# Optimization experiments

Hardware: AMD Instinct MI355X
Metric: run time of the kernel (lower is better)

Reference implementation:

```python
import math
import jax, jax.numpy as jnp
import numpy as np

FNUM = 64      # exp_channels (fnum)
NHEADS = 4     # num_heads
WS = 8         # window size (both spatial dims)
SHIFT = 4      # cyclic shift (hard-coded in module)
SCALE = FNUM ** -0.5   # NOTE: module scales by fnum**-0.5, not head_dim**-0.5
LN_EPS = 1e-5


def sine_pos_encoding(h, w, num_pos_feats, temperature=10000.0):
    # DETR-style normalized sine position encoding -> (1, h*w, 2*num_pos_feats)
    scale = 2.0 * math.pi
    y = np.cumsum(np.ones((1, h, w), dtype=np.float64), axis=1)
    x = np.cumsum(np.ones((1, h, w), dtype=np.float64), axis=2)
    eps = 1e-6
    y = y / (y[:, -1:, :] + eps) * scale
    x = x / (x[:, :, -1:] + eps) * scale
    dim_t = np.arange(num_pos_feats, dtype=np.float64)
    dim_t = temperature ** (2.0 * (dim_t // 2) / num_pos_feats)
    pos_x = x[..., None] / dim_t
    pos_y = y[..., None] / dim_t
    pos_x = np.stack([np.sin(pos_x[..., 0::2]), np.cos(pos_x[..., 1::2])], axis=-1).reshape(1, h, w, -1)
    pos_y = np.stack([np.sin(pos_y[..., 0::2]), np.cos(pos_y[..., 1::2])], axis=-1).reshape(1, h, w, -1)
    pos = np.concatenate([pos_y, pos_x], axis=-1)
    return jnp.asarray(pos.reshape(1, h * w, 2 * num_pos_feats), dtype=jnp.float32)


def compute_mask_np(H, W, ws, ss):
    # Swin shifted-window attention mask -> (nW, ws*ws, ws*ws) with 0 / -100
    img = np.zeros((H, W))
    cnt = 0
    for hs in (slice(0, -ws), slice(-ws, -ss), slice(-ss, None)):
        for wsl in (slice(0, -ws), slice(-ws, -ss), slice(-ss, None)):
            img[hs, wsl] = cnt
            cnt += 1
    mw = img.reshape(H // ws, ws, W // ws, ws).transpose(0, 2, 1, 3).reshape(-1, ws * ws)
    diff = mw[:, None, :] - mw[:, :, None]
    return jnp.asarray(np.where(diff != 0, -100.0, 0.0), dtype=jnp.float32)


def layernorm(x, w, b):
    m = x.mean(-1, keepdims=True)
    v = x.var(-1, keepdims=True)
    return (x - m) * jax.lax.rsqrt(v + LN_EPS) * w + b


def window_attention(q, k, v, mask):
    # q,k,v: (Bw, nH, N, Ch); mask: (nW, N, N)
    att = jnp.einsum('bhnc,bhmc->bhnm', q * SCALE, k)
    nW, N = mask.shape[0], mask.shape[1]
    att = att.reshape(-1, nW, NHEADS, N, N) + mask[None, :, None]
    att = jax.nn.softmax(att.reshape(-1, NHEADS, N, N), axis=-1)
    out = jnp.einsum('bhnm,bhmc->bnhc', att, v)   # merge heads as (nH C)
    return out.reshape(out.shape[0], N, -1)


def merge_heads(q):
    # (Bw, nH, N, Ch) -> (Bw, N, nH*Ch)
    return q.transpose(0, 2, 1, 3).reshape(q.shape[0], q.shape[2], -1)


def geglu(h, w11, b11, w12, b12, w2, b2):
    return (jax.nn.gelu(h @ w11 + b11, approximate=False) * (h @ w12 + b12)) @ w2 + b2


def reference(x, ln1_w, ln1_b, ln2_w, ln2_b, w_qkv, me_w11, me_b11, me_w12, me_b12, me_w2, me_b2, conv11_w, ff_in_w, ff_dw_w, ff_out_w):
    B, _, C, H, W = x.shape
    nHw, nWw = H // WS, W // WS
    nW = nHw * nWw
    N = WS * WS
    Ch = FNUM // NHEADS
    pos = sine_pos_encoding(WS, WS, FNUM // 2)
    mask = compute_mask_np(H, W, WS, SHIFT)
    x0 = x
    xs = jnp.roll(x, (-SHIFT, -SHIFT), axis=(3, 4))
    # window partition: (B,3,C,H,W) -> (B*3*nW, N, C)
    xw = xs.reshape(B, 3, C, nHw, WS, nWw, WS).transpose(0, 1, 3, 5, 4, 6, 2).reshape(-1, N, C)
    xw = layernorm(xw, ln1_w, ln1_b)
    qkv = (xw + pos) @ w_qkv                                   # (B*3*nW, N, 3F)
    # '(B E nW) W (nP C) -> E nP (B nW) W C'
    qkv = qkv.reshape(B, 3, nW, N, 3, FNUM).transpose(1, 4, 0, 2, 3, 5).reshape(3, 3, B * nW, N, FNUM)
    # '(C nH)' head split: head index is the fast axis (faithful to source)
    qkv = qkv.reshape(3, 3, B * nW, N, Ch, NHEADS).transpose(0, 1, 2, 5, 3, 4)  # (E, P, Bw, nH, N, Ch)
    a1 = window_attention(qkv[1, 0], qkv[0, 1], qkv[0, 2], mask)
    a3 = window_attention(qkv[1, 0], qkv[2, 1], qkv[2, 2], mask)
    a21 = window_attention(qkv[0, 0], qkv[1, 1], qkv[1, 2], mask)
    a21b = window_attention(qkv[0, 0], qkv[2, 1], qkv[2, 2], mask)
    a23 = window_attention(qkv[2, 0], qkv[1, 1], qkv[1, 2], mask)
    a23b = window_attention(qkv[2, 0], qkv[0, 1], qkv[0, 2], mask)
    # keep_query=True path: concat attended features with own query, GEGLU per exposure
    h1 = geglu(jnp.concatenate([a21, a21b, merge_heads(qkv[0, 0])], -1), me_w11[0], me_b11[0], me_w12[0], me_b12[0], me_w2[0], me_b2[0])
    h2 = geglu(jnp.concatenate([a1, a3, merge_heads(qkv[1, 0])], -1), me_w11[1], me_b11[1], me_w12[1], me_b12[1], me_w2[1], me_b2[1])
    h3 = geglu(jnp.concatenate([a23, a23b, merge_heads(qkv[2, 0])], -1), me_w11[2], me_b11[2], me_w12[2], me_b12[2], me_w2[2], me_b2[2])
    xc = jnp.concatenate([h1, h2, h3], 0)                      # (3*B*nW, N, F)
    # window reverse + ffn_dconv 1x1 conv across 3F channels
    xr = xc.reshape(3, B, nHw, nWw, WS, WS, FNUM).transpose(1, 0, 6, 2, 4, 3, 5).reshape(B, 3 * FNUM, H, W)
    xr = jnp.einsum('oi,bihw->bohw', conv11_w, xr).reshape(B, 3, FNUM, H, W)
    xr = jnp.roll(xr, (SHIFT, SHIFT), axis=(3, 4))
    xres = xr + x0
    # FFN: LN over (N C), then GEGLU dwconv FeedForward
    xl = layernorm(xres.transpose(0, 3, 4, 1, 2).reshape(B, H, W, 3 * FNUM), ln2_w, ln2_b)
    xcn = xl.transpose(0, 3, 1, 2)                             # (B, 3F, H, W)
    h = jnp.einsum('oi,bihw->bohw', ff_in_w, xcn)              # (B, 12F, H, W)
    h = jax.lax.conv_general_dilated(h, ff_dw_w[:, None], (1, 1), ((1, 1), (1, 1)),
                                     feature_group_count=h.shape[1],
                                     dimension_numbers=('NCHW', 'OIHW', 'NCHW'))
    g1, g2 = jnp.split(h, 2, axis=1)
    h = jax.nn.gelu(g1, approximate=False) * g2                # (B, 6F, H, W)
    out = jnp.einsum('oi,bihw->bohw', ff_out_w, h).reshape(B, 3, FNUM, H, W)
    return xres + out


def setup_inputs():
    key = jax.random.key(0)
    ks = jax.random.split(key, 10)
    F3, F6, F12 = 3 * FNUM, 6 * FNUM, 12 * FNUM
    def w(k, shape, fan_in):
        return jax.random.normal(k, shape, jnp.float32) * (fan_in ** -0.5)
    return {
        'x': jax.random.normal(ks[0], (1, 3, FNUM, 256, 256), jnp.float32),
        'ln1_w': jnp.ones((FNUM,), jnp.float32),
        'ln1_b': jnp.zeros((FNUM,), jnp.float32),
        'ln2_w': jnp.ones((F3,), jnp.float32),
        'ln2_b': jnp.zeros((F3,), jnp.float32),
        'w_qkv': w(ks[1], (FNUM, F3), FNUM),
        'me_w11': w(ks[2], (3, F3, FNUM), F3),
        'me_b11': jnp.zeros((3, FNUM), jnp.float32),
        'me_w12': w(ks[3], (3, F3, FNUM), F3),
        'me_b12': jnp.zeros((3, FNUM), jnp.float32),
        'me_w2': w(ks[4], (3, FNUM, FNUM), FNUM),
        'me_b2': jnp.zeros((3, FNUM), jnp.float32),
        'conv11_w': w(ks[5], (F3, F3), F3),
        'ff_in_w': w(ks[6], (F12, F3), F3),
        'ff_dw_w': w(ks[7], (F12, 3, 3), 9),
        'ff_out_w': w(ks[8], (F3, F6), F6),
    }
```

## Files before the change

### kernel.cpp

```cpp
#include <hip/hip_runtime.h>
#include <hip/hip_bf16.h>
#include <math.h>

typedef __hip_bfloat16 bf16;
typedef __attribute__((ext_vector_type(8))) short short8;
typedef __attribute__((ext_vector_type(4))) short short4v;
typedef __attribute__((ext_vector_type(4))) float f32x4;

__device__ __forceinline__ float b2f(bf16 v) { return __bfloat162float(v); }
__device__ __forceinline__ bf16 f2b(float v) { return __float2bfloat16(v); }
__device__ __forceinline__ short f2s(float v) { bf16 b = __float2bfloat16(v); return *(short*)&b; }
__device__ __forceinline__ float s2f(short s) { bf16 b = *(bf16*)&s; return __bfloat162float(b); }
__device__ __forceinline__ float gelu_fast(float x) {
  float z = 0.7978845608028654f * x * (1.0f + 0.044715f * x * x);
  float e = __expf(2.0f * z);
  float t = 1.0f - 2.0f / (e + 1.0f);
  return 0.5f * x * (1.0f + t);
}
__device__ __forceinline__ bool detect_f32(const void* ln1w) {
  return *(const unsigned int*)ln1w == 0x3F800000u;
}
__device__ __forceinline__ float ldx(const void* p, int i, bool f32) {
  return f32 ? ((const float*)p)[i] : b2f(((const bf16*)p)[i]);
}
#define MFMA16(a, b, c) __builtin_amdgcn_mfma_f32_16x16x32_bf16((a), (b), (c), 0, 0, 0)

#define OFF_LN1W  0
#define OFF_LN1B  64
#define OFF_LN2W  128
#define OFF_LN2B  320
#define OFF_WQKVT 512
#define OFF_W11T  12800
#define OFF_B11   49664
#define OFF_W12T  49856
#define OFF_B12   86720
#define OFF_W2T   86912
#define OFF_B2    99200
#define OFF_CW    99392
#define OFF_FIW   136256
#define OFF_DWW   283712
#define OFF_FOW   290624

#define QOFF 0
#define KOFF 4352
#define VOFF 9472

__global__ void __launch_bounds__(256) k_convert(
    const void* __restrict__ src, bf16* __restrict__ dst, int n,
    const void* __restrict__ raw) {
  const bool f32 = detect_f32(raw);
  int i = blockIdx.x * 256 + threadIdx.x;
  if (i < n) dst[i] = f2b(ldx(src, i, f32));
}

__global__ void __launch_bounds__(256) k_convT(
    const void* __restrict__ src, bf16* __restrict__ dst, int R, int C, int n,
    const void* __restrict__ raw) {
  const bool f32 = detect_f32(raw);
  int i = blockIdx.x * 256 + threadIdx.x;
  if (i >= n) return;
  int rc = R * C;
  int s = i / rc, rem = i - s * rc;
  int r = rem / C, c = rem - r * C;
  dst[s * rc + c * R + r] = f2b(ldx(src, i, f32));
}

__global__ void __launch_bounds__(256) k_pos(float* __restrict__ posT) {
  int i = blockIdx.x * 256 + threadIdx.x;
  if (i >= 4096) return;
  int t = i >> 6, ch = i & 63;
  int r = t >> 3, c = t & 7;
  int c2 = ch & 31;
  float coord = (ch < 32) ? (float)(r + 1) : (float)(c + 1);
  float base = coord * (6.283185307179586f / 8.000001f);
  int k = c2 >> 1;
  float d = powf(10000.0f, (float)k * (1.0f / 16.0f));
  float a = base / d;
  posT[i] = (c2 & 1) ? cosf(a) : sinf(a);
}

__global__ void __launch_bounds__(256) k_qkv(
    const void* __restrict__ x, const void* __restrict__ raw,
    const bf16* __restrict__ W, const float* __restrict__ posT,
    short* __restrict__ qkvS, int wy0, int NWL) {
  const int wl = blockIdx.x;
  const int wy = wy0 + (wl >> 5), wx = wl & 31;
  const int tid = threadIdx.x;
  const bool xf32 = detect_f32(raw);

  __shared__ alignas(16) short xln[192 * 72];
  __shared__ alignas(16) short qout[13824];
  __shared__ float mu[192], rs[192];

  for (int i = tid; i < 3072; i += 256) {
    int xq = i & 1, ty = (i >> 1) & 7, ch = (i >> 4) & 63, e = i >> 10;
    int y  = (wy * 8 + ty + 4) & 255;
    int xs = (wx * 8 + 4 + xq * 4) & 255;
    size_t gi = ((size_t)(e * 64 + ch) * 256 + y) * 256 + xs;
    float f0, f1, f2, f3;
    if (xf32) {
      f32x4 v4 = *(const f32x4*)((const float*)x + gi);
      f0 = v4[0]; f1 = v4[1]; f2 = v4[2]; f3 = v4[3];
    } else {
      short4v v4 = *(const short4v*)((const bf16*)x + gi);
      f0 = s2f(v4[0]); f1 = s2f(v4[1]); f2 = s2f(v4[2]); f3 = s2f(v4[3]);
    }
    int tb = (e * 64 + ty * 8 + xq * 4) * 72 + ch;
    xln[tb]       = f2s(f0);
    xln[tb + 72]  = f2s(f1);
    xln[tb + 144] = f2s(f2);
    xln[tb + 216] = f2s(f3);
  }
  __syncthreads();
  if (tid < 192) {
    const short* row = xln + tid * 72;
    float s = 0.f, s2 = 0.f;
    #pragma unroll
    for (int k8 = 0; k8 < 8; k8++) {
      short8 v = *(const short8*)(row + k8 * 8);
      #pragma unroll
      for (int j = 0; j < 8; j++) { float f = s2f(v[j]); s += f; s2 += f * f; }
    }
    float m = s * (1.0f / 64.0f);
    float var = s2 * (1.0f / 64.0f) - m * m;
    mu[tid] = m; rs[tid] = rsqrtf(var + 1e-5f);
  }
  __syncthreads();
  for (int u = tid; u < 1536; u += 256) {
    int co = u & 7, t = (u >> 3) & 63, e = u >> 9;
    int idx = (e * 64 + t) * 72 + co * 8;
    short8 xv = *(const short8*)(xln + idx);
    float m = mu[e * 64 + t], rr = rs[e * 64 + t];
    const float* pt = posT + t * 64 + co * 8;
    f32x4 pa = *(const f32x4*)pt;
    f32x4 pb = *(const f32x4*)(pt + 4);
    short8 lw = *(const short8*)(const void*)(W + OFF_LN1W + co * 8);
    short8 lb = *(const short8*)(const void*)(W + OFF_LN1B + co * 8);
    short8 o;
    #pragma unroll
    for (int j = 0; j < 8; j++) {
      float p = (j < 4) ? pa[j] : pb[j - 4];
      o[j] = f2s((s2f(xv[j]) - m) * rr * s2f(lw[j]) + s2f(lb[j]) + p);
    }
    *(short8*)(xln + idx) = o;
  }
  __syncthreads();

  const int lid = tid & 63;
  const int w = tid >> 6;
  const int mrow = lid & 15, q = lid >> 4;
  const int t0 = w * 16 + q * 4;
  const int h = mrow & 3;
  const bf16* wqT = W + OFF_WQKVT;
  for (int e = 0; e < 3; e++) {
    short8 a0 = *(const short8*)(xln + (e * 64 + w * 16 + mrow) * 72 + q * 8);
    short8 a1 = *(const short8*)(xln + (e * 64 + w * 16 + mrow) * 72 + 32 + q * 8);
    for (int nt = 0; nt < 12; nt++) {
      f32x4 acc = {0.f, 0.f, 0.f, 0.f};
      short8 b0 = *(const short8*)(const void*)(wqT + (nt * 16 + mrow) * 64 + q * 8);
      short8 b1 = *(const short8*)(const void*)(wqT + (nt * 16 + mrow) * 64 + 32 + q * 8);
      acc = MFMA16(a0, b0, acc);
      acc = MFMA16(a1, b1, acc);
      int p = nt >> 2;
      int c = (nt & 3) * 4 + (mrow >> 2);
      if (p == 0) {
        int o2 = h * 16 + c;
        #pragma unroll
        for (int r = 0; r < 4; r++)
          qout[QOFF + (t0 + r) * 68 + o2] = f2s(acc[r]);
      } else if (p == 1) {
        int rb = KOFF + (h * 64 + t0) * 20 + c;
        #pragma unroll
        for (int r = 0; r < 4; r++)
          qout[rb + r * 20] = f2s(acc[r] * 0.125f);
      } else {
        int rb = VOFF + (h * 16 + c) * 68 + q * 16 + w;
        #pragma unroll
        for (int r = 0; r < 4; r++)
          qout[rb + r * 4] = f2s(acc[r]);
      }
    }
    __syncthreads();
    const size_t gb = ((size_t)wl * 9 + e * 3) * 4096;
    for (int u = tid; u < 3072; u += 256) {
      int j = u * 4, p = j >> 12, rem = j & 4095, src;
      if (p == 0)      src = QOFF + (rem >> 6) * 68 + (rem & 63);
      else if (p == 1) src = KOFF + (rem >> 4) * 20 + (rem & 15);
      else             src = VOFF + (rem >> 6) * 68 + (rem & 63);
      *(short4v*)(qkvS + gb + j) = *(const short4v*)(qout + src);
    }
    __syncthreads();
  }
}

__global__ void __launch_bounds__(256, 3) k_attn(
    const short* __restrict__ qkvS, const bf16* __restrict__ W,
    short* __restrict__ xcS, int wy0, int NWL) {
  const int e  = blockIdx.x / NWL;
  const int wl = blockIdx.x - e * NWL;
  const int wy = wy0 + (wl >> 5), wx = wl & 31;
  const int tid = threadIdx.x;

  __shared__ alignas(16) short cat[64 * 200];
  __shared__ alignas(16) short Kh[4096];
  __shared__ alignas(16) short Vt[64 * 72];
  __shared__ alignas(16) short Pb[64 * 72];
  __shared__ alignas(16) short kz[16];
  short* gbuf = Pb;

  const int ea = (e == 0) ? 1 : ((e == 1) ? 0 : 1);
  const int eb = (e == 0) ? 2 : ((e == 1) ? 2 : 0);
  const short* Qg = qkvS + ((size_t)wl * 9 + e * 3 + 0) * 4096;
  const short* Kg[2] = { qkvS + ((size_t)wl * 9 + ea * 3 + 1) * 4096,
                         qkvS + ((size_t)wl * 9 + eb * 3 + 1) * 4096 };
  const short* Vg[2] = { qkvS + ((size_t)wl * 9 + ea * 3 + 2) * 4096,
                         qkvS + ((size_t)wl * 9 + eb * 3 + 2) * 4096 };

  if (tid < 16) kz[tid] = 0;
  for (int i = tid; i < 512; i += 256) {
    int t = i >> 3, ch = i & 7;
    *(short8*)(cat + t * 200 + 128 + ch * 8) = *(const short8*)(Qg + t * 64 + ch * 8);
  }

  const int lid = tid & 63;
  const int w = tid >> 6;
  const int mrow = lid & 15, q = lid >> 4;
  const int masky = (wy == 31), maskx = (wx == 31);
  const bool anymask = (masky | maskx) != 0;
  const short8 zero8 = {0, 0, 0, 0, 0, 0, 0, 0};

  float madd[4][4];
  if (anymask) {
    int qi = w * 16 + mrow;
    int lyi = masky ? (((qi >> 3) < 4) ? 1 : 2) : 0;
    int lxi = maskx ? (((qi & 7) < 4) ? 1 : 2) : 0;
    #pragma unroll
    for (int nt = 0; nt < 4; nt++)
      #pragma unroll
      for (int r = 0; r < 4; r++) {
        int kj = nt * 16 + q * 4 + r;
        int lyj = masky ? (((kj >> 3) < 4) ? 1 : 2) : 0;
        int lxj = maskx ? (((kj & 7) < 4) ? 1 : 2) : 0;
        madd[nt][r] = (lyi != lyj || lxi != lxj) ? -100.0f : 0.0f;
      }
  }

  for (int src = 0; src < 2; src++) {
    if (src) __syncthreads();
    for (int i = tid; i < 512; i += 256)
      *(short8*)(Kh + i * 8) = *(const short8*)(Kg[src] + i * 8);
    for (int i = tid; i < 512; i += 256) {
      int row = i >> 3, ch = i & 7;
      *(short8*)(Vt + row * 72 + ch * 8) = *(const short8*)(Vg[src] + row * 64 + ch * 8);
    }
    __syncthreads();

    for (int h = 0; h < 4; h++) {
      short8 qf = (q < 2)
          ? *(const short8*)(cat + (w * 16 + mrow) * 200 + 128 + h * 16 + q * 8)
          : zero8;
      const short* kb; int kstep;
      if (q < 2) { kb = Kh + (h * 64 + mrow) * 16 + q * 8; kstep = 256; }
      else       { kb = kz; kstep = 0; }
      f32x4 s[4];
      #pragma unroll
      for (int nt = 0; nt < 4; nt++) {
        short8 kf = *(const short8*)(kb + nt * kstep);
        f32x4 z = {0.f, 0.f, 0.f, 0.f};
        s[nt] = MFMA16(kf, qf, z);
      }
      if (anymask) {
        #pragma unroll
        for (int nt = 0; nt < 4; nt++)
          #pragma unroll
          for (int r = 0; r < 4; r++) s[nt][r] += madd[nt][r];
      }
      float mx = s[0][0];
      #pragma unroll
      for (int nt = 0; nt < 4; nt++)
        #pragma unroll
        for (int r = 0; r < 4; r++) if (nt | r) mx = fmaxf(mx, s[nt][r]);
      mx = fmaxf(mx, __shfl_xor(mx, 16));
      mx = fmaxf(mx, __shfl_xor(mx, 32));
      float pr[4][4]; float sum = 0.f;
      #pragma unroll
      for (int nt = 0; nt < 4; nt++)
        #pragma unroll
        for (int r = 0; r < 4; r++) {
          float ev = __expf(s[nt][r] - mx);
          pr[nt][r] = ev; sum += ev;
        }
      sum += __shfl_xor(sum, 16);
      sum += __shfl_xor(sum, 32);
      float inv = 1.0f / sum;
      int ro = (w * 16 + mrow) * 72 + q * 16;
      #pragma unroll
      for (int r = 0; r < 4; r++) {
        short4v pv = { f2s(pr[0][r] * inv), f2s(pr[1][r] * inv),
                       f2s(pr[2][r] * inv), f2s(pr[3][r] * inv) };
        *(short4v*)(Pb + ro + r * 4) = pv;
      }
      asm volatile("s_waitcnt lgkmcnt(0)" ::: "memory");
      f32x4 o = {0.f, 0.f, 0.f, 0.f};
      #pragma unroll
      for (int kc = 0; kc < 2; kc++) {
        short8 pa = *(const short8*)(Pb + (w * 16 + mrow) * 72 + kc * 32 + q * 8);
        short8 vb = *(const short8*)(Vt + (h * 16 + mrow) * 72 + kc * 32 + q * 8);
        o = MFMA16(pa, vb, o);
      }
      #pragma unroll
      for (int r = 0; r < 4; r++)
        cat[(w * 16 + q * 4 + r) * 200 + src * 64 + h * 16 + mrow] = f2s(o[r]);
    }
  }
  __syncthreads();

  {
    short8 a[6];
    #pragma unroll
    for (int kc = 0; kc < 6; kc++)
      a[kc] = *(const short8*)(cat + (w * 16 + mrow) * 200 + kc * 32 + q * 8);
    f32x4 ua[4], va[4];
    const bf16* w1T = W + OFF_W11T + (size_t)e * 64 * 192;
    const bf16* w2T = W + OFF_W12T + (size_t)e * 64 * 192;
    for (int nt = 0; nt < 4; nt++) {
      f32x4 au = {0.f, 0.f, 0.f, 0.f}, av = {0.f, 0.f, 0.f, 0.f};
      #pragma unroll
      for (int kc = 0; kc < 6; kc++) {
        short8 bu = *(const short8*)(const void*)(w1T + (nt * 16 + mrow) * 192 + kc * 32 + q * 8);
        short8 bv = *(const short8*)(const void*)(w2T + (nt * 16 + mrow) * 192 + kc * 32 + q * 8);
        au = MFMA16(a[kc], bu, au);
        av = MFMA16(a[kc], bv, av);
      }
      ua[nt] = au; va[nt] = av;
    }
    for (int nt = 0; nt < 4; nt++) {
      int o = nt * 16 + mrow;
      float bu = b2f(W[OFF_B11 + e * 64 + o]);
      float bv = b2f(W[OFF_B12 + e * 64 + o]);
      #pragma unroll
      for (int r = 0; r < 4; r++)
        gbuf[(w * 16 + q * 4 + r) * 72 + o] = f2s(gelu_fast(ua[nt][r] + bu) * (va[nt][r] + bv));
    }
  }
  {
    short8 g0 = *(const short8*)(gbuf + (w * 16 + mrow) * 72 + q * 8);
    short8 g1 = *(const short8*)(gbuf + (w * 16 + mrow) * 72 + 32 + q * 8);
    const bf16* w2T = W + OFF_W2T + (size_t)e * 64 * 64;
    for (int nt = 0; nt < 4; nt++) {
      f32x4 acc = {0.f, 0.f, 0.f, 0.f};
      short8 b0 = *(const short8*)(const void*)(w2T + (nt * 16 + mrow) * 64 + q * 8);
      short8 b1 = *(const short8*)(const void*)(w2T + (nt * 16 + mrow) * 64 + 32 + q * 8);
      acc = MFMA16(g0, b0, acc);
      acc = MFMA16(g1, b1, acc);
      int o = nt * 16 + mrow;
      float bb = b2f(W[OFF_B2 + e * 64 + o]);
      #pragma unroll
      for (int r = 0; r < 4; r++)
        cat[(w * 16 + q * 4 + r) * 200 + o] = f2s(acc[r] + bb);
    }
  }
  __syncthreads();
  short* xcbase = xcS + ((size_t)wl * 3 + e) * 4096;
  for (int i = tid; i < 1024; i += 256) {
    int tt = i >> 4, f4 = (i & 15) * 4;
    *(short4v*)(xcbase + tt * 64 + f4) = *(const short4v*)(cat + tt * 200 + f4);
  }
}

__global__ void __launch_bounds__(256) k_conv11(
    const short* __restrict__ xcS, const bf16* __restrict__ W,
    const void* __restrict__ x, const void* __restrict__ raw,
    short* __restrict__ xres, int wy0, int NWL) {
  const int wl = blockIdx.x;
  const int wy = wy0 + (wl >> 5), wx = wl & 31;
  const int tid = threadIdx.x;
  const bool xf32 = detect_f32(raw);
  __shared__ alignas(16) short ct[64 * 200];
  __shared__ alignas(16) short xt[64 * 200];

  for (int i = tid; i < 3072; i += 256) {
    int e = i >> 10, rem = i & 1023;
    int tt = rem >> 4, f4 = (rem & 15) * 4;
    *(short4v*)(ct + tt * 200 + e * 64 + f4)
        = *(const short4v*)(xcS + ((size_t)wl * 3 + e) * 4096 + tt * 64 + f4);
  }
  for (int i = tid; i < 3072; i += 256) {
    int xq = i & 1, ty = (i >> 1) & 7, ch = (i >> 4) & 63, e = i >> 10;
    int y  = (wy * 8 + ty + 4) & 255;
    int xs = (wx * 8 + 4 + xq * 4) & 255;
    size_t gi = ((size_t)(e * 64 + ch) * 256 + y) * 256 + xs;
    float f0, f1, f2, f3;
    if (xf32) {
      f32x4 v4 = *(const f32x4*)((const float*)x + gi);
      f0 = v4[0]; f1 = v4[1]; f2 = v4[2]; f3 = v4[3];
    } else {
      short4v v4 = *(const short4v*)((const bf16*)x + gi);
      f0 = s2f(v4[0]); f1 = s2f(v4[1]); f2 = s2f(v4[2]); f3 = s2f(v4[3]);
    }
    int tb = (ty * 8 + xq * 4) * 200 + e * 64 + ch;
    xt[tb]       = f2s(f0);
    xt[tb + 200] = f2s(f1);
    xt[tb + 400] = f2s(f2);
    xt[tb + 600] = f2s(f3);
  }
  __syncthreads();

  const int lid = tid & 63;
  const int w = tid >> 6;
  const int mrow = lid & 15, q = lid >> 4;
  short8 a[6];
  #pragma unroll
  for (int kc = 0; kc < 6; kc++)
    a[kc] = *(const short8*)(ct + (w * 16 + mrow) * 200 + kc * 32 + q * 8);
  __syncthreads();

  const bf16* cw = W + OFF_CW;
  for (int nt = 0; nt < 12; nt++) {
    f32x4 acc = {0.f, 0.f, 0.f, 0.f};
    #pragma unroll
    for (int kc = 0; kc < 6; kc++) {
      short8 b = *(const short8*)(const void*)(cw + (nt * 16 + mrow) * 192 + kc * 32 + q * 8);
      acc = MFMA16(a[kc], b, acc);
    }
    int o = nt * 16 + mrow;
    #pragma unroll
    for (int r = 0; r < 4; r++) {
      int t = w * 16 + q * 4 + r;
      ct[t * 200 + o] = f2s(acc[r] + s2f(xt[t * 200 + o]));
    }
  }
  __syncthreads();
  for (int i4 = tid; i4 < 3072; i4 += 256) {
    int t = i4 / 48, o4 = (i4 - t * 48) * 4;
    int y  = (wy * 8 + (t >> 3) + 4) & 255;
    int xx = (wx * 8 + (t & 7) + 4) & 255;
    *(short4v*)(xres + (size_t)(y * 256 + xx) * 192 + o4)
        = *(const short4v*)(ct + t * 200 + o4);
  }
}

__global__ void __launch_bounds__(256) k_ffin(
    const short* __restrict__ xres, const bf16* __restrict__ W,
    short* __restrict__ hS, int y_start, int y0m1) {
  const int y = y_start + (blockIdx.x >> 2);
  const int x0 = (blockIdx.x & 3) * 64;
  const int l = y - y0m1;
  const int tid = threadIdx.x;
  __shared__ alignas(16) short xt[64 * 200];
  __shared__ float mu[64], rs[64];

  for (int i4 = tid; i4 < 3072; i4 += 256) {
    int p = i4 / 48, c4 = (i4 - p * 48) * 4;
    *(short4v*)(xt + p * 200 + c4)
        = *(const short4v*)(xres + (size_t)(y * 256 + x0 + p) * 192 + c4);
  }
  __syncthreads();
  {
    int p = tid >> 2, qd = tid & 3;
    const short* row = xt + p * 200 + qd * 48;
    float s = 0.f, s2 = 0.f;
    #pragma unroll
    for (int k = 0; k < 6; k++) {
      short8 v = *(const short8*)(row + k * 8);
      #pragma unroll
      for (int j = 0; j < 8; j++) { float f = s2f(v[j]); s += f; s2 += f * f; }
    }
    s  += __shfl_xor(s, 1);  s  += __shfl_xor(s, 2);
    s2 += __shfl_xor(s2, 1); s2 += __shfl_xor(s2, 2);
    if (qd == 0) {
      float m = s * (1.0f / 192.0f);
      float var = s2 * (1.0f / 192.0f) - m * m;
      mu[p] = m; rs[p] = rsqrtf(var + 1e-5f);
    }
  }
  __syncthreads();
  for (int i = tid; i < 12288; i += 256) {
    int p = i & 63, ch = i >> 6;
    int idx = p * 200 + ch;
    xt[idx] = f2s((s2f(xt[idx]) - mu[p]) * rs[p] * b2f(W[OFF_LN2W + ch]) + b2f(W[OFF_LN2B + ch]));
  }
  __syncthreads();

  const int lid = tid & 63;
  const int m0 = (tid >> 6) * 16;
  const int mrow = lid & 15, q = lid >> 4;
  short8 a[6];
  #pragma unroll
  for (int kc = 0; kc < 6; kc++)
    a[kc] = *(const short8*)(xt + (m0 + mrow) * 200 + kc * 32 + q * 8);
  __syncthreads();

  const bf16* fiw = W + OFF_FIW;
  for (int c = 0; c < 4; c++) {
    for (int j = 0; j < 12; j++) {
      int nt = c * 12 + j;
      f32x4 acc = {0.f, 0.f, 0.f, 0.f};
      #pragma unroll
      for (int kc = 0; kc < 6; kc++) {
        short8 b = *(const short8*)(const void*)(fiw + (nt * 16 + mrow) * 192 + kc * 32 + q * 8);
        acc = MFMA16(a[kc], b, acc);
      }
      #pragma unroll
      for (int r = 0; r < 4; r++)
        xt[(m0 + q * 4 + r) * 200 + j * 16 + mrow] = f2s(acc[r]);
    }
    __syncthreads();
    for (int i4 = tid; i4 < 3072; i4 += 256) {
      int t = i4 / 48, o4 = (i4 - t * 48) * 4;
      *(short4v*)(hS + (size_t)l * 196608 + (size_t)(x0 + t) * 768 + c * 192 + o4)
          = *(const short4v*)(xt + t * 200 + o4);
    }
    __syncthreads();
  }
}

__global__ void __launch_bounds__(256) k_ffout(
    const short* __restrict__ hS, const bf16* __restrict__ W,
    const short* __restrict__ xres, void* __restrict__ out,
    const void* __restrict__ raw, int y0, int y0m1) {
  const int y = y0 + (blockIdx.x >> 2);
  const int x0 = (blockIdx.x & 3) * 64;
  const int tid = threadIdx.x;
  const bool of32 = detect_f32(raw);
  __shared__ alignas(16) short ga[64 * 392];

  const bf16* dwwT = W + OFF_DWW;
  const int l = y - y0m1;
  const short8 z8 = {0, 0, 0, 0, 0, 0, 0, 0};
  for (int it = 0; it < 6; it++) {
    int unit = it * 256 + tid;
    int pq = unit / 48, oo = unit - pq * 48;
    int o = oo * 8;
    int xxb = x0 + pq * 2;
    float u0[8] = {0,0,0,0,0,0,0,0}, v0[8] = {0,0,0,0,0,0,0,0};
    float u1[8] = {0,0,0,0,0,0,0,0}, v1[8] = {0,0,0,0,0,0,0,0};
    #pragma unroll
    for (int dy = -1; dy <= 1; dy++) {
      int yy = y + dy;
      if (yy < 0 || yy >= 256) continue;
      const short* rbase = hS + (size_t)(l + dy) * 196608;
      short8 hu[4], hv[4];
      #pragma unroll
      for (int k = 0; k < 4; k++) {
        int xv = xxb - 1 + k;
        if (xv < 0 || xv >= 256) { hu[k] = z8; hv[k] = z8; }
        else {
          const short* hp = rbase + (size_t)xv * 768 + o;
          hu[k] = *(const short8*)(hp);
          hv[k] = *(const short8*)(hp + 384);
        }
      }
      const bf16* wrow = dwwT + (dy + 1) * 3 * 768 + o;
      short8 w0u = *(const short8*)(const void*)(wrow);
      short8 w0v = *(const short8*)(const void*)(wrow + 384);
      short8 w1u = *(const short8*)(const void*)(wrow + 768);
      short8 w1v = *(const short8*)(const void*)(wrow + 768 + 384);
      short8 w2u = *(const short8*)(const void*)(wrow + 1536);
      short8 w2v = *(const short8*)(const void*)(wrow + 1536 + 384);
      #pragma unroll
      for (int j = 0; j < 8; j++) {
        float a0 = s2f(w0u[j]), a1 = s2f(w1u[j]), a2 = s2f(w2u[j]);
        float b0 = s2f(w0v[j]), b1 = s2f(w1v[j]), b2 = s2f(w2v[j]);
        float h0u = s2f(hu[0][j]), h1u = s2f(hu[1][j]), h2u = s2f(hu[2][j]), h3u = s2f(hu[3][j]);
        float h0v = s2f(hv[0][j]), h1v = s2f(hv[1][j]), h2v = s2f(hv[2][j]), h3v = s2f(hv[3][j]);
        u0[j] += a0 * h0u + a1 * h1u + a2 * h2u;
        u1[j] += a0 * h1u + a1 * h2u + a2 * h3u;
        v0[j] += b0 * h0v + b1 * h1v + b2 * h2v;
        v1[j] += b0 * h1v + b1 * h2v + b2 * h3v;
      }
    }
    short8 g0, g1;
    #pragma unroll
    for (int j = 0; j < 8; j++) {
      g0[j] = f2s(gelu_fast(u0[j]) * v0[j]);
      g1[j] = f2s(gelu_fast(u1[j]) * v1[j]);
    }
    *(short8*)(ga + (pq * 2) * 392 + o)     = g0;
    *(short8*)(ga + (pq * 2 + 1) * 392 + o) = g1;
  }
  __syncthreads();

  const int lid = tid & 63;
  const int m0 = (tid >> 6) * 16;
  const int mrow = lid & 15, q = lid >> 4;
  short8 a[12];
  #pragma unroll
  for (int kc = 0; kc < 12; kc++)
    a[kc] = *(const short8*)(ga + (m0 + mrow) * 392 + kc * 32 + q * 8);
  __syncthreads();

  for (int i4 = tid; i4 < 3072; i4 += 256) {
    int pp = i4 / 48, c4 = (i4 - pp * 48) * 4;
    *(short4v*)(ga + pp * 392 + 200 + c4)
        = *(const short4v*)(xres + (size_t)(y * 256 + x0 + pp) * 192 + c4);
  }

  const bf16* fow = W + OFF_FOW;
  for (int nt = 0; nt < 12; nt++) {
    f32x4 acc = {0.f, 0.f, 0.f, 0.f};
    #pragma unroll
    for (int kc = 0; kc < 12; kc++) {
      short8 b = *(const short8*)(const void*)(fow + (nt * 16 + mrow) * 384 + kc * 32 + q * 8);
      acc = MFMA16(a[kc], b, acc);
    }
    #pragma unroll
    for (int r = 0; r < 4; r++)
      ga[(m0 + q * 4 + r) * 392 + nt * 16 + mrow] = f2s(acc[r]);
  }
  __syncthreads();

  for (int it = 0; it < 48; it++) {
    int flat = it * 256 + tid;
    int pp = flat & 63, ch = flat >> 6;
    int idx = ch * 65536 + y * 256 + x0 + pp;
    float r = s2f(ga[pp * 392 + ch]) + s2f(ga[pp * 392 + 200 + ch]);
    if (of32) ((float*)out)[idx] = r;
    else      ((bf16*)out)[idx] = f2b(r);
  }
}

extern "C" void kernel_launch(void* const* d_in, const int* in_sizes, int n_in,
                              void* d_out, int out_size, void* d_ws, size_t ws_size,
                              hipStream_t stream) {
  const void* x   = d_in[0];
  const void* raw = d_in[1];
  char* ws = (char*)d_ws;
  bf16*  W    = (bf16*)(ws + 1024);
  float* posT = (float*)(ws + 786432);
  short* xres = (short*)(ws + 0x100000);
  const size_t ATT = 28ull * 1024 * 1024;

  size_t avail = (ws_size > ATT) ? ws_size - ATT : 0;
  int swr = 32;
  while (swr > 1 && (size_t)swr * 3145728ull > avail) swr >>= 1;
  int hr = 256;
  while (hr > 4 && (size_t)(hr + 2) * 393216ull > avail) hr >>= 1;

  short* qkvS = (short*)(ws + ATT);
  short* xcS  = (short*)(ws + ATT + (size_t)swr * 2359296ull);
  short* hS   = (short*)(ws + ATT);

  { const int di[10]   = {1, 2, 3, 4, 7, 9, 11, 12, 13, 15};
    const int offp[10] = {OFF_LN1W, OFF_LN1B, OFF_LN2W, OFF_LN2B, OFF_B11,
                          OFF_B12, OFF_B2, OFF_CW, OFF_FIW, OFF_FOW};
    const int cnt[10]  = {64, 64, 192, 192, 192, 192, 192, 36864, 147456, 73728};
    for (int i = 0; i < 10; i++)
      k_convert<<<(cnt[i] + 255) / 256, 256, 0, stream>>>(
          d_in[di[i]], W + offp[i], cnt[i], raw);
  }
  k_convT<<<(12288 + 255) / 256, 256, 0, stream>>>(d_in[5], W + OFF_WQKVT, 64, 192, 12288, raw);
  k_convT<<<(36864 + 255) / 256, 256, 0, stream>>>(d_in[6], W + OFF_W11T, 192, 64, 36864, raw);
  k_convT<<<(36864 + 255) / 256, 256, 0, stream>>>(d_in[8], W + OFF_W12T, 192, 64, 36864, raw);
  k_convT<<<(12288 + 255) / 256, 256, 0, stream>>>(d_in[10], W + OFF_W2T, 64, 64, 12288, raw);
  k_convT<<<(6912 + 255) / 256, 256, 0, stream>>>(d_in[14], W + OFF_DWW, 768, 9, 6912, raw);
  k_pos<<<16, 256, 0, stream>>>(posT);

  for (int wy0 = 0; wy0 < 32; wy0 += swr) {
    int NWL = swr * 32;
    k_qkv<<<NWL, 256, 0, stream>>>(x, raw, W, posT, qkvS, wy0, NWL);
    k_attn<<<3 * NWL, 256, 0, stream>>>(qkvS, W, xcS, wy0, NWL);
    k_conv11<<<NWL, 256, 0, stream>>>(xcS, W, x, raw, xres, wy0, NWL);
  }

  for (int y0 = 0; y0 < 256; y0 += hr) {
    int ys = (y0 == 0) ? 0 : (y0 - 1);
    int ye = (y0 + hr > 255) ? 255 : (y0 + hr);
    int nrows = ye - ys + 1;
    k_ffin<<<nrows * 4, 256, 0, stream>>>(xres, W, hS, ys, y0 - 1);
    k_ffout<<<hr * 4, 256, 0, stream>>>(hS, W, xres, d_out, raw, y0, y0 - 1);
  }
}
```

Before: 704.4 us.

## Swap MFMA operands to store GEMM outputs directly to global, skipping LDS staging

In the output-projection and FFN-input kernels, the MFMA operands are swapped so each lane holds four consecutive output channels for one pixel. Those lanes can then write short4 vectors straight to global memory, which removes the LDS round-trip, the extra copy loops and several __syncthreads. The LN2 normalization loop is also vectorized to 8-wide loads. The cost is global stores spread over more scattered rows, which may coalesce less well than the previous staged copy.

```diff
diff --git a/kernel.cpp b/kernel.cpp
--- a/kernel.cpp
+++ b/kernel.cpp
@@ -413,7 +413,12 @@
   #pragma unroll
   for (int kc = 0; kc < 6; kc++)
     a[kc] = *(const short8*)(ct + (w * 16 + mrow) * 200 + kc * 32 + q * 8);
-  __syncthreads();
+
+  const int t = w * 16 + mrow;
+  const int ty2 = (wy * 8 + (t >> 3) + 4) & 255;
+  const int tx2 = (wx * 8 + (t & 7) + 4) & 255;
+  short* xrow = xres + (size_t)(ty2 * 256 + tx2) * 192;
+  const short* resrow = xt + t * 200;
 
   const bf16* cw = W + OFF_CW;
   for (int nt = 0; nt < 12; nt++) {
@@ -421,22 +426,13 @@
     #pragma unroll
     for (int kc = 0; kc < 6; kc++) {
       short8 b = *(const short8*)(const void*)(cw + (nt * 16 + mrow) * 192 + kc * 32 + q * 8);
-      acc = MFMA16(a[kc], b, acc);
-    }
-    int o = nt * 16 + mrow;
-    #pragma unroll
-    for (int r = 0; r < 4; r++) {
-      int t = w * 16 + q * 4 + r;
-      ct[t * 200 + o] = f2s(acc[r] + s2f(xt[t * 200 + o]));
-    }
-  }
-  __syncthreads();
-  for (int i4 = tid; i4 < 3072; i4 += 256) {
-    int t = i4 / 48, o4 = (i4 - t * 48) * 4;
-    int y  = (wy * 8 + (t >> 3) + 4) & 255;
-    int xx = (wx * 8 + (t & 7) + 4) & 255;
-    *(short4v*)(xres + (size_t)(y * 256 + xx) * 192 + o4)
-        = *(const short4v*)(ct + t * 200 + o4);
+      acc = MFMA16(b, a[kc], acc);
+    }
+    int o = nt * 16 + q * 4;
+    short4v rv = *(const short4v*)(resrow + o);
+    short4v o4 = { f2s(acc[0] + s2f(rv[0])), f2s(acc[1] + s2f(rv[1])),
+                   f2s(acc[2] + s2f(rv[2])), f2s(acc[3] + s2f(rv[3])) };
+    *(short4v*)(xrow + o) = o4;
   }
 }
 
@@ -475,10 +471,18 @@
     }
   }
   __syncthreads();
-  for (int i = tid; i < 12288; i += 256) {
-    int p = i & 63, ch = i >> 6;
-    int idx = p * 200 + ch;
-    xt[idx] = f2s((s2f(xt[idx]) - mu[p]) * rs[p] * b2f(W[OFF_LN2W + ch]) + b2f(W[OFF_LN2B + ch]));
+  for (int u = tid; u < 1536; u += 256) {
+    int p = u / 24, c8 = u - p * 24;
+    int idx = p * 200 + c8 * 8;
+    short8 xv = *(const short8*)(xt + idx);
+    float m = mu[p], rr = rs[p];
+    short8 lw = *(const short8*)(const void*)(W + OFF_LN2W + c8 * 8);
+    short8 lb = *(const short8*)(const void*)(W + OFF_LN2B + c8 * 8);
+    short8 o;
+    #pragma unroll
+    for (int j = 0; j < 8; j++)
+      o[j] = f2s((s2f(xv[j]) - m) * rr * s2f(lw[j]) + s2f(lb[j]));
+    *(short8*)(xt + idx) = o;
   }
   __syncthreads();
 
@@ -489,29 +493,18 @@
   #pragma unroll
   for (int kc = 0; kc < 6; kc++)
     a[kc] = *(const short8*)(xt + (m0 + mrow) * 200 + kc * 32 + q * 8);
-  __syncthreads();
 
   const bf16* fiw = W + OFF_FIW;
-  for (int c = 0; c < 4; c++) {
-    for (int j = 0; j < 12; j++) {
-      int nt = c * 12 + j;
-      f32x4 acc = {0.f, 0.f, 0.f, 0.f};
-      #pragma unroll
-      for (int kc = 0; kc < 6; kc++) {
-        short8 b = *(const short8*)(const void*)(fiw + (nt * 16 + mrow) * 192 + kc * 32 + q * 8);
-        acc = MFMA16(a[kc], b, acc);
-      }
-      #pragma unroll
-      for (int r = 0; r < 4; r++)
-        xt[(m0 + q * 4 + r) * 200 + j * 16 + mrow] = f2s(acc[r]);
-    }
-    __syncthreads();
-    for (int i4 = tid; i4 < 3072; i4 += 256) {
-      int t = i4 / 48, o4 = (i4 - t * 48) * 4;
-      *(short4v*)(hS + (size_t)l * 196608 + (size_t)(x0 + t) * 768 + c * 192 + o4)
-          = *(const short4v*)(xt + t * 200 + o4);
-    }
-    __syncthreads();
+  short* hrow = hS + (size_t)l * 196608 + (size_t)(x0 + m0 + mrow) * 768;
+  for (int nt = 0; nt < 48; nt++) {
+    f32x4 acc = {0.f, 0.f, 0.f, 0.f};
+    #pragma unroll
+    for (int kc = 0; kc < 6; kc++) {
+      short8 b = *(const short8*)(const void*)(fiw + (nt * 16 + mrow) * 192 + kc * 32 + q * 8);
+      acc = MFMA16(b, a[kc], acc);
+    }
+    short4v o4 = { f2s(acc[0]), f2s(acc[1]), f2s(acc[2]), f2s(acc[3]) };
+    *(short4v*)(hrow + nt * 16 + q * 4) = o4;
   }
 }
 
```

Measured after the change: 705.8 us. About the same (+0.2%).
